# Optimization experiments

Measured on AMD Instinct MI355X. Metric: run time of the kernel, lower is better.

## Reference

```python
import jax, jax.numpy as jnp
import numpy as np

N = 50000          # nodes
E = 1_600_000      # edges (avg degree 32)
F = 64             # num_features == hidden dim of every layer
R = 5              # num_rel (edge ratings)
B = 4              # num_base (basis decomposition)
L = 4              # number of RGCN layers (dim=[64,64,64,64])
K = 2048           # nodes with x[:,0]==1 (target user/item nodes)


def setup_inputs() -> dict:
    key = jax.random.key(0)
    ks = jax.random.split(key, 10)
    x = jax.random.normal(ks[0], (N, F), dtype=jnp.float32)
    target_idx = jnp.arange(K, dtype=jnp.int32)
    # mark exactly K target nodes: x[:,0] == 1 iff node index < K
    col0 = (jnp.arange(N) < K).astype(jnp.float32)
    x = x.at[:, 0].set(col0)
    edge_index = jax.random.randint(ks[1], (2, E), 0, N, dtype=jnp.int32)
    edge_type = jax.random.randint(ks[2], (E,), 0, R, dtype=jnp.int32)
    s = 1.0 / np.sqrt(F)
    bases = jax.random.normal(ks[3], (L, B, F, F), dtype=jnp.float32) * s
    comps = jax.random.normal(ks[4], (L, R, B), dtype=jnp.float32) * (1.0 / np.sqrt(B))
    roots = jax.random.normal(ks[5], (L, F, F), dtype=jnp.float32) * s
    biases = jnp.zeros((L, F), dtype=jnp.float32)
    w1 = jax.random.normal(ks[6], (2 * L * F, 128), dtype=jnp.float32) * (1.0 / np.sqrt(2 * L * F))
    b1 = jnp.zeros((128,), dtype=jnp.float32)
    w2 = jax.random.normal(ks[7], (128, 1), dtype=jnp.float32) * (1.0 / np.sqrt(128))
    b2 = jnp.zeros((1,), dtype=jnp.float32)
    return {"x": x, "edge_index": edge_index, "edge_type": edge_type,
            "target_idx": target_idx, "bases": bases, "comps": comps,
            "roots": roots, "biases": biases, "w1": w1, "b1": b1,
            "w2": w2, "b2": b2}


def _rgcn_layer(x, src, dst, etype, bases_l, comp_l, root_l, bias_l):
    # basis decomposition: W_r = sum_b comp[r,b] * bases[b]   -> [R, in, out]
    W = jnp.einsum('rb,bio->rio', comp_l, bases_l)
    # transform every node under every relation, then gather per edge
    H = jnp.einsum('ni,rio->rno', x, W)          # [R, N, out]
    m = H[etype, src]                            # [E, out] per-edge messages
    # per-(target node, relation) MEAN aggregation (PyG RGCNConv semantics)
    seg = dst * R + etype                        # [E]
    sums = jax.ops.segment_sum(m, seg, num_segments=N * R)
    cnts = jax.ops.segment_sum(jnp.ones((m.shape[0],), dtype=x.dtype), seg,
                               num_segments=N * R)
    mean = sums / jnp.maximum(cnts, 1.0)[:, None]
    agg = mean.reshape(N, R, -1).sum(axis=1)     # sum over relations
    return agg + x @ root_l + bias_l


def reference(x, edge_index, edge_type, target_idx, bases, comps, roots,
              biases, w1, b1, w2, b2):
    # inference mode: edge dropout / feature dropout are identity
    src, dst = edge_index[0], edge_index[1]
    h = x
    h_i = []
    for l in range(L):
        h = jnp.tanh(_rgcn_layer(h, src, dst, edge_type,
                                 bases[l], comps[l], roots[l], biases[l]))
        h_i.append(h)
    h_cat = jnp.concatenate(h_i, axis=1)         # [N, sum(dim)] = [N, 256]
    # u and i masks are identical in the source (x[:,0]==1); target_idx holds
    # exactly those node indices, so index gather == boolean mask selection.
    sel = h_cat[target_idx]                      # [K, 256]
    feat = jnp.concatenate([sel, sel], axis=1)   # [K, 512]
    hid = jax.nn.relu(feat @ w1 + b1)
    out = hid @ w2 + b2
    return out[:, 0]
```

## Files before the change

kernel.cpp:

```cpp
#include <hip/hip_runtime.h>
#include <hip/hip_bf16.h>

#define Nn 50000
#define Ee 1600000
#define Ff 64
#define Rr 5
#define Bb 4
#define Ll 4
#define Kk 2048
#define NBK 196
#define SEGB 1280
#define MsegP (NBK*SEGB)
#define NT16 3125
#define NCH ((Ee+8191)/8192)
#define WTSL (12*4*64*8)

typedef __attribute__((ext_vector_type(8))) short short8;
typedef __attribute__((ext_vector_type(4))) float v4f;

static __device__ __forceinline__ unsigned short f2b(float f){
  unsigned u = __float_as_uint(f);
  unsigned r = (u + 0x7fffu + ((u>>16)&1u)) >> 16;
  return (unsigned short)r;
}
static __device__ __forceinline__ unsigned packbf(float lo, float hi){
  return (unsigned)f2b(lo) | ((unsigned)f2b(hi) << 16);
}
static __device__ __forceinline__ float2 unpackbf(unsigned u){
  return make_float2(__uint_as_float(u << 16), __uint_as_float(u & 0xffff0000u));
}

#define XB_B 6250
#define IV_B (XB_B+196)
#define WE_B (IV_B+128)
#define WS_B (WE_B+48)
#define TF_B (WS_B+13)
#define MS_B (TF_B+1)
__global__ __launch_bounds__(256) void k_setupA(const float* __restrict__ x, unsigned* __restrict__ xb,
    int* __restrict__ inv, const float* __restrict__ w1, float* __restrict__ w1e,
    const float* __restrict__ bases, const float* __restrict__ comps, const float* __restrict__ roots,
    unsigned short* __restrict__ WTs, int* __restrict__ t16f, int* __restrict__ bcnt,
    unsigned* __restrict__ hA, unsigned* __restrict__ hB)
{
  int b = blockIdx.x, t = threadIdx.x;
  if (b < XB_B){
    int idx = b*256 + t;
    int n = idx >> 5, j = idx & 31;
    float2 v = *(const float2*)&x[(size_t)n*64 + 2*j];
    xb[idx] = packbf(v.x, v.y);
  } else if (b < IV_B){
    int i = (b-XB_B)*256 + t;
    if (i < Nn) inv[i] = -1;
  } else if (b < WE_B){
    int idx = (b-IV_B)*256 + t;
    int i = idx >> 7, j = idx & 127;
    w1e[idx] = w1[i*128 + j] + w1[(i+256)*128 + j];
  } else if (b < WS_B){
    int gid = (b-WE_B)*256 + t;
    int lane = gid & 63, nb = (gid>>6)&3, idx2 = gid>>8;
    int l = idx2/12, kk = idx2 - l*12;
    int o = nb*16 + (lane & 15);
    int kbase = kk*32 + (lane>>4)*8;
    const float* basesl = bases + (size_t)l*Bb*Ff*Ff;
    const float* compsl = comps + (size_t)l*Rr*Bb;
    const float* rootsl = roots + (size_t)l*Ff*Ff;
    unsigned short* wp = WTs + (size_t)gid*8;
    #pragma unroll
    for (int j=0;j<8;j++){
      int k = kbase + j;
      float s;
      if (k < 320){
        int c = k >> 6, i = k & 63;
        s = 0.f;
        #pragma unroll
        for (int bb2=0;bb2<Bb;bb2++)
          s += compsl[c*Bb+bb2] * basesl[(bb2*Ff + i)*Ff + o];
      } else {
        s = rootsl[(k-320)*Ff + o];
      }
      wp[j] = f2b(s);
    }
  } else if (b < TF_B){
    int i = (b-WS_B)*256 + t;
    if (i < NT16) t16f[i] = 0;
  } else {
    if (t < NBK+1) bcnt[t] = 0;
    if (t < 32){
      xb[(size_t)Nn*32 + t] = 0;
      hA[(size_t)Nn*32 + t] = 0;
      hB[(size_t)Nn*32 + t] = 0;
    }
  }
}

__global__ __launch_bounds__(256) void k_setupB(const int* __restrict__ tidx, int* __restrict__ inv,
                                                int* __restrict__ t16f){
  int k = blockIdx.x*256+threadIdx.x;
  if (k < Kk){
    int n = tidx[k];
    inv[n] = k;
    t16f[n >> 4] = 1;
  }
}

__global__ __launch_bounds__(256) void k_bcnt(const int* __restrict__ ei, int* __restrict__ bcnt){
  __shared__ int h[NBK];
  int t = threadIdx.x;
  for (int i=t;i<NBK;i+=256) h[i]=0;
  __syncthreads();
  int base = blockIdx.x*8192;
  for (int i=0;i<32;i++){
    int e = base + i*256 + t;
    if (e < Ee) atomicAdd(&h[ei[Ee+e]>>8], 1);
  }
  __syncthreads();
  for (int i=t;i<NBK;i+=256) if (h[i]) atomicAdd(&bcnt[i], h[i]);
}

__global__ __launch_bounds__(256) void k_bscan(const int* __restrict__ bcnt, int* __restrict__ bbase,
                                               int* __restrict__ bfill, int* __restrict__ rowptr){
  __shared__ int s[256];
  int t = threadIdx.x;
  int v = (t < NBK) ? bcnt[t] : 0;
  s[t] = v; __syncthreads();
  #pragma unroll
  for (int off=1; off<256; off<<=1){
    int x = (t>=off) ? s[t-off] : 0;
    __syncthreads();
    s[t] += x;
    __syncthreads();
  }
  if (t < NBK){ int ex = s[t]-v; bbase[t]=ex; bfill[t]=ex; }
  if (t == 0){ bbase[NBK] = Ee; rowptr[MsegP] = Ee; }
}

__global__ __launch_bounds__(256) void k_bin(const int* __restrict__ ei, const int* __restrict__ et,
                                             int* __restrict__ bfill, unsigned* __restrict__ ebin){
  __shared__ unsigned led[8192];
  __shared__ int h[NBK], gb[NBK];
  int t = threadIdx.x;
  for (int i=t;i<NBK;i+=256) h[i]=0;
  __syncthreads();
  int base = blockIdx.x*8192;
  for (int i=0;i<32;i++){
    int e = base + i*256 + t;
    if (e < Ee){
      int src = ei[e];
      int dst = ei[Ee+e];
      int r = et[e];
      led[i*256+t] = (unsigned)src | ((unsigned)(dst&255)<<16) | ((unsigned)r<<24);
      atomicAdd(&h[dst>>8], 1);
    }
  }
  __syncthreads();
  for (int i=t;i<NBK;i+=256) if (h[i]){ gb[i] = atomicAdd(&bfill[i], h[i]); h[i] = 0; }
  __syncthreads();
  for (int i=0;i<32;i++){
    int e = base + i*256 + t;
    if (e < Ee){
      int b = ei[Ee+e]>>8;
      int off = atomicAdd(&h[b], 1);
      ebin[gb[b]+off] = led[i*256+t];
    }
  }
}

__global__ __launch_bounds__(512) void k_sort(const unsigned* __restrict__ ebin, const int* __restrict__ bbase,
                                              unsigned short* __restrict__ srcs, int* __restrict__ rowptr){
  __shared__ int cntA[SEGB], excA[SEGB];
  int b = blockIdx.x, t = threadIdx.x;
  int base = bbase[b], cnt = bbase[b+1]-base;
  for (int i=t;i<SEGB;i+=512) cntA[i]=0;
  __syncthreads();
  for (int i=t;i<cnt;i+=512){
    unsigned u = ebin[base+i];
    int segl = (int)((u>>24)&7u)*256 + (int)((u>>16)&255u);
    atomicAdd(&cntA[segl], 1);
  }
  __syncthreads();
  for (int i=t;i<SEGB;i+=512) excA[i]=cntA[i];
  __syncthreads();
  for (int off=1; off<SEGB; off<<=1){
    int i0=t, i1=t+512, i2=t+1024;
    int v0 = (i0>=off)? excA[i0-off] : 0;
    int v1 = (i1>=off)? excA[i1-off] : 0;
    int v2 = (i2<SEGB && i2>=off)? excA[i2-off] : 0;
    __syncthreads();
    excA[i0]+=v0;
    excA[i1]+=v1;
    if (i2<SEGB) excA[i2]+=v2;
    __syncthreads();
  }
  for (int i=t;i<SEGB;i+=512){
    int ex = excA[i]-cntA[i];
    excA[i] = ex;
    rowptr[b*SEGB+i] = base + ex;
    cntA[i] = 0;
  }
  __syncthreads();
  for (int i=t;i<cnt;i+=512){
    unsigned u = ebin[base+i];
    int segl = (int)((u>>24)&7u)*256 + (int)((u>>16)&255u);
    int off = atomicAdd(&cntA[segl], 1);
    srcs[base + excA[segl] + off] = (unsigned short)(u & 0xffffu);
  }
}

static __device__ __forceinline__ void gpass(int mys, float* A, int p, int half5, int sub, int li,
                                             const unsigned* __restrict__ h2)
{
  int s0 = __shfl(mys, half5 + p +      sub, 64);
  int s1 = __shfl(mys, half5 + p +  4 + sub, 64);
  int s2 = __shfl(mys, half5 + p +  8 + sub, 64);
  int s3 = __shfl(mys, half5 + p + 12 + sub, 64);
  uint4 g0 = *(const uint4*)&h2[(size_t)s0*32 + li*4];
  uint4 g1 = *(const uint4*)&h2[(size_t)s1*32 + li*4];
  uint4 g2 = *(const uint4*)&h2[(size_t)s2*32 + li*4];
  uint4 g3 = *(const uint4*)&h2[(size_t)s3*32 + li*4];
  float2 f;
  f=unpackbf(g0.x); A[0]+=f.x; A[1]+=f.y;  f=unpackbf(g0.y); A[2]+=f.x; A[3]+=f.y;
  f=unpackbf(g0.z); A[4]+=f.x; A[5]+=f.y;  f=unpackbf(g0.w); A[6]+=f.x; A[7]+=f.y;
  f=unpackbf(g1.x); A[0]+=f.x; A[1]+=f.y;  f=unpackbf(g1.y); A[2]+=f.x; A[3]+=f.y;
  f=unpackbf(g1.z); A[4]+=f.x; A[5]+=f.y;  f=unpackbf(g1.w); A[6]+=f.x; A[7]+=f.y;
  f=unpackbf(g2.x); A[0]+=f.x; A[1]+=f.y;  f=unpackbf(g2.y); A[2]+=f.x; A[3]+=f.y;
  f=unpackbf(g2.z); A[4]+=f.x; A[5]+=f.y;  f=unpackbf(g2.w); A[6]+=f.x; A[7]+=f.y;
  f=unpackbf(g3.x); A[0]+=f.x; A[1]+=f.y;  f=unpackbf(g3.y); A[2]+=f.x; A[3]+=f.y;
  f=unpackbf(g3.z); A[4]+=f.x; A[5]+=f.y;  f=unpackbf(g3.w); A[6]+=f.x; A[7]+=f.y;
}

static __device__ __forceinline__ void tail_gather(float* A, int s, int e, int li,
    const unsigned short* __restrict__ srcs, const unsigned* __restrict__ h2)
{
  for (int i = s; i < e; i++){
    uint4 g = *(const uint4*)&h2[(size_t)srcs[i]*32 + li*4];
    float2 f;
    f=unpackbf(g.x); A[0]+=f.x; A[1]+=f.y;  f=unpackbf(g.y); A[2]+=f.x; A[3]+=f.y;
    f=unpackbf(g.z); A[4]+=f.x; A[5]+=f.y;  f=unpackbf(g.w); A[6]+=f.x; A[7]+=f.y;
  }
}

__global__ __launch_bounds__(256, 4) void k_fused(const unsigned short* __restrict__ srcs,
    const int* __restrict__ rowptr, const unsigned* __restrict__ h2,
    const unsigned short* __restrict__ WTsl, const float* __restrict__ bias,
    unsigned short* __restrict__ hn, const int* __restrict__ inv, float* __restrict__ sel,
    int layer, const int* __restrict__ t16f)
{
  if (layer == Ll-1 && t16f[blockIdx.x] == 0) return;
  __shared__ __align__(16) unsigned short ytile[5*16*64];
  char* yb = (char*)ytile;
  int tid = threadIdx.x;
  int hw = tid >> 5;
  int l2 = tid & 31, li = l2 & 7, sub = l2 >> 3;
  int half5 = tid & 32;
  int wl = tid & 63;
  int d0 = blockIdx.x * 16;
  int sbase = (d0 >> 8)*SEGB + (d0 & 255) + hw*2;
  int rl0 = hw*2;

  #pragma unroll 1
  for (int r = 0; r < Rr; ++r){
    int sA = sbase + r*256;
    int2 pp = *(const int2*)&rowptr[sA];
    int p2 = rowptr[sA+2];
    int degA = pp.y - pp.x, degB = p2 - pp.y;
    unsigned ldA = srcs[pp.x + l2];
    unsigned ldB = srcs[pp.y + l2];
    int mysA = (l2 < degA) ? (int)ldA : Nn;
    int mysB = (l2 < degB) ? (int)ldB : Nn;
    float aA[8] = {0.f,0.f,0.f,0.f,0.f,0.f,0.f,0.f};
    float aB[8] = {0.f,0.f,0.f,0.f,0.f,0.f,0.f,0.f};

    gpass(mysA, aA, 0, half5, sub, li, h2);
    gpass(mysB, aB, 0, half5, sub, li, h2);
    if (degA > 16) gpass(mysA, aA, 16, half5, sub, li, h2);
    if (degB > 16) gpass(mysB, aB, 16, half5, sub, li, h2);
    if (sub == 0){
      if (degA > 32) tail_gather(aA, pp.x+32, pp.y, li, srcs, h2);
      if (degB > 32) tail_gather(aB, pp.y+32, p2,   li, srcs, h2);
    }
    #pragma unroll
    for (int k=0;k<8;k++){
      aA[k] += __shfl(aA[k], wl^8, 64);
      aB[k] += __shfl(aB[k], wl^8, 64);
    }
    #pragma unroll
    for (int k=0;k<8;k++){
      aA[k] += __shfl(aA[k], wl^16, 64);
      aB[k] += __shfl(aB[k], wl^16, 64);
    }
    if (sub == 0){
      float scA = (degA > 0) ? 1.0f/(float)degA : 0.f;
      float scB = (degB > 0) ? 1.0f/(float)degB : 0.f;
      uint4 oA, oB;
      oA.x = packbf(aA[0]*scA, aA[1]*scA);
      oA.y = packbf(aA[2]*scA, aA[3]*scA);
      oA.z = packbf(aA[4]*scA, aA[5]*scA);
      oA.w = packbf(aA[6]*scA, aA[7]*scA);
      oB.x = packbf(aB[0]*scB, aB[1]*scB);
      oB.y = packbf(aB[2]*scB, aB[3]*scB);
      oB.z = packbf(aB[4]*scB, aB[5]*scB);
      oB.w = packbf(aB[6]*scB, aB[7]*scB);
      int trA = r*16 + rl0;
      *(uint4*)(yb + (( trA   *128 + li*16) ^ (( rl0   &7)<<4))) = oA;
      *(uint4*)(yb + (((trA+1)*128 + li*16) ^ (((rl0+1)&7)<<4))) = oB;
    }
  }
  __syncthreads();

  int wv = tid >> 6;
  int lane = tid & 63;
  int m = lane & 15, q = lane >> 4;
  const unsigned short* wp = WTsl + (size_t)lane*8 + (size_t)wv*512;
  const char* h2c = (const char*)h2;
  int rowm = d0 + m;
  v4f acc = {0.f,0.f,0.f,0.f};
  #pragma unroll
  for (int kk=0; kk<12; kk++){
    short8 a;
    if (kk < 10){
      int tr = (kk>>1)*16 + m;
      a = *(const short8*)(yb + ((tr*128 + (kk&1)*64 + q*16) ^ ((m&7)<<4)));
    } else {
      a = *(const short8*)(h2c + (size_t)rowm*128 + (size_t)(kk&1)*64 + q*16);
    }
    short8 bf = *(const short8*)(wp + (size_t)kk*2048);
    acc = __builtin_amdgcn_mfma_f32_16x16x32_bf16(a, bf, acc, 0, 0, 0);
  }
  float bc = bias[wv*16 + m];
  #pragma unroll
  for (int j=0;j<4;j++){
    int node = d0 + q*4 + j;
    float rres = tanhf(acc[j] + bc);
    if (layer != Ll-1)
      hn[(size_t)node*64 + wv*16 + m] = f2b(rres);
    int k = inv[node];
    if (k >= 0)
      sel[(size_t)k*256 + layer*64 + wv*16 + m] = rres;
  }
}

__global__ __launch_bounds__(128) void k_mlp(const float* __restrict__ sel, const float* __restrict__ w1e,
    const float* __restrict__ b1, const float* __restrict__ w2, const float* __restrict__ b2,
    float* __restrict__ out)
{
  __shared__ float sfeat[256];
  __shared__ float partial[2];
  int k = blockIdx.x, j = threadIdx.x;
  for (int idx=j; idx<256; idx+=128) sfeat[idx] = sel[(size_t)k*256 + idx];
  __syncthreads();
  float a = b1[j];
  for (int i=0;i<256;i++) a += sfeat[i] * w1e[i*128 + j];
  a = fmaxf(a, 0.f);
  float v = a * w2[j];
  #pragma unroll
  for (int off=32; off>0; off>>=1) v += __shfl_down(v, off, 64);
  if ((j & 63) == 0) partial[j>>6] = v;
  __syncthreads();
  if (j == 0) out[k] = partial[0] + partial[1] + b2[0];
}

extern "C" void kernel_launch(void* const* d_in, const int* in_sizes, int n_in,
                              void* d_out, int out_size, void* d_ws, size_t ws_size,
                              hipStream_t stream){
  const float* x     = (const float*)d_in[0];
  const int*  ei     = (const int*)d_in[1];
  const int*  et     = (const int*)d_in[2];
  const int*  tidx   = (const int*)d_in[3];
  const float* bases = (const float*)d_in[4];
  const float* comps = (const float*)d_in[5];
  const float* roots = (const float*)d_in[6];
  const float* biases= (const float*)d_in[7];
  const float* w1    = (const float*)d_in[8];
  const float* b1    = (const float*)d_in[9];
  const float* w2    = (const float*)d_in[10];
  const float* b2    = (const float*)d_in[11];
  float* out = (float*)d_out;

  char* wsp = (char*)d_ws;
  size_t off = 0;
  auto alloc = [&](size_t bytes)->void*{ void* p = wsp + off; off += (bytes + 255) & ~size_t(255); return p; };
  unsigned* xb    = (unsigned*)alloc(sizeof(unsigned)*((size_t)Nn+1)*32);
  unsigned* hA    = (unsigned*)alloc(sizeof(unsigned)*((size_t)Nn+1)*32);
  unsigned* hB    = (unsigned*)alloc(sizeof(unsigned)*((size_t)Nn+1)*32);
  unsigned* ebin  = (unsigned*)alloc(sizeof(unsigned)*(size_t)Ee);
  int*      bcnt  = (int*)  alloc(sizeof(int)*(NBK+1));
  int*      bbase = (int*)  alloc(sizeof(int)*(NBK+1));
  int*      bfill = (int*)  alloc(sizeof(int)*(NBK));
  int*      rowptr= (int*)  alloc(sizeof(int)*(MsegP+1));
  unsigned short* srcs = (unsigned short*)alloc(sizeof(unsigned short)*((size_t)Ee+64));
  unsigned short* WTs  = (unsigned short*)alloc(sizeof(unsigned short)*(size_t)Ll*WTSL);
  float*    sel   = (float*)alloc(sizeof(float)*(size_t)Kk*256);
  float*    w1e   = (float*)alloc(sizeof(float)*256*128);
  int*      inv   = (int*)  alloc(sizeof(int)*(size_t)Nn);
  int*      t16f  = (int*)  alloc(sizeof(int)*NT16);
  (void)ws_size;

  k_setupA<<<MS_B+1, 256, 0, stream>>>(x, xb, inv, w1, w1e, bases, comps, roots,
                                       WTs, t16f, bcnt, hA, hB);
  k_setupB<<<(Kk+255)/256, 256, 0, stream>>>(tidx, inv, t16f);
  k_bcnt<<<NCH, 256, 0, stream>>>(ei, bcnt);
  k_bscan<<<1, 256, 0, stream>>>(bcnt, bbase, bfill, rowptr);
  k_bin<<<NCH, 256, 0, stream>>>(ei, et, bfill, ebin);
  k_sort<<<NBK, 512, 0, stream>>>(ebin, bbase, srcs, rowptr);

  const unsigned* hc = xb;
  unsigned* hn = hA;
  for (int l=0;l<Ll;l++){
    k_fused<<<NT16, 256, 0, stream>>>(srcs, rowptr, hc, WTs + (size_t)l*WTSL,
                                      biases + (size_t)l*Ff, (unsigned short*)hn,
                                      inv, sel, l, t16f);
    hc = hn;
    hn = (hn == hA) ? hB : hA;
  }
  k_mlp<<<Kk, 128, 0, stream>>>(sel, w1e, b1, w2, b2, out);
}
```

Before: 322.2 us.

## Process 32 nodes per block with 8-lane segment gathers and dual MFMA tiles

The fused RGCN layer kernel now handles 32 destination nodes per block instead of 16. Each (node, relation) segment is gathered by an 8-lane group instead of a 32-lane group with cross-lane reductions, so no shuffle-reduction is needed. The epilogue issues two MFMA tiles that share each weight fragment load, halving the number of blocks and the per-node weight traffic. The catch is loop divergence: each group iterates to the wave's maximum degree, and the doubled shared tile may lower occupancy. Bounds checks are added for the partial last block.

```diff
diff --git a/kernel.cpp b/kernel.cpp
--- a/kernel.cpp
+++ b/kernel.cpp
@@ -11,7 +11,7 @@
 #define NBK 196
 #define SEGB 1280
 #define MsegP (NBK*SEGB)
-#define NT16 3125
+#define NT32 1563
 #define NCH ((Ee+8191)/8192)
 #define WTSL (12*4*64*8)
 
@@ -29,17 +29,23 @@
 static __device__ __forceinline__ float2 unpackbf(unsigned u){
   return make_float2(__uint_as_float(u << 16), __uint_as_float(u & 0xffff0000u));
 }
+static __device__ __forceinline__ void acc8(float* A, uint4 g){
+  float2 f;
+  f=unpackbf(g.x); A[0]+=f.x; A[1]+=f.y;
+  f=unpackbf(g.y); A[2]+=f.x; A[3]+=f.y;
+  f=unpackbf(g.z); A[4]+=f.x; A[5]+=f.y;
+  f=unpackbf(g.w); A[6]+=f.x; A[7]+=f.y;
+}
 
 #define XB_B 6250
 #define IV_B (XB_B+196)
 #define WE_B (IV_B+128)
 #define WS_B (WE_B+48)
-#define TF_B (WS_B+13)
-#define MS_B (TF_B+1)
+#define TF_B (WS_B+7)
 __global__ __launch_bounds__(256) void k_setupA(const float* __restrict__ x, unsigned* __restrict__ xb,
     int* __restrict__ inv, const float* __restrict__ w1, float* __restrict__ w1e,
     const float* __restrict__ bases, const float* __restrict__ comps, const float* __restrict__ roots,
-    unsigned short* __restrict__ WTs, int* __restrict__ t16f, int* __restrict__ bcnt,
+    unsigned short* __restrict__ WTs, int* __restrict__ t32f, int* __restrict__ bcnt,
     unsigned* __restrict__ hA, unsigned* __restrict__ hB)
 {
   int b = blockIdx.x, t = threadIdx.x;
@@ -82,7 +88,7 @@
     }
   } else if (b < TF_B){
     int i = (b-WS_B)*256 + t;
-    if (i < NT16) t16f[i] = 0;
+    if (i < NT32) t32f[i] = 0;
   } else {
     if (t < NBK+1) bcnt[t] = 0;
     if (t < 32){
@@ -94,12 +100,12 @@
 }
 
 __global__ __launch_bounds__(256) void k_setupB(const int* __restrict__ tidx, int* __restrict__ inv,
-                                                int* __restrict__ t16f){
+                                                int* __restrict__ t32f){
   int k = blockIdx.x*256+threadIdx.x;
   if (k < Kk){
     int n = tidx[k];
     inv[n] = k;
-    t16f[n >> 4] = 1;
+    t32f[n >> 5] = 1;
   }
 }
 
@@ -206,104 +212,81 @@
   }
 }
 
-static __device__ __forceinline__ void gpass(int mys, float* A, int p, int half5, int sub, int li,
-                                             const unsigned* __restrict__ h2)
-{
-  int s0 = __shfl(mys, half5 + p +      sub, 64);
-  int s1 = __shfl(mys, half5 + p +  4 + sub, 64);
-  int s2 = __shfl(mys, half5 + p +  8 + sub, 64);
-  int s3 = __shfl(mys, half5 + p + 12 + sub, 64);
-  uint4 g0 = *(const uint4*)&h2[(size_t)s0*32 + li*4];
-  uint4 g1 = *(const uint4*)&h2[(size_t)s1*32 + li*4];
-  uint4 g2 = *(const uint4*)&h2[(size_t)s2*32 + li*4];
-  uint4 g3 = *(const uint4*)&h2[(size_t)s3*32 + li*4];
-  float2 f;
-  f=unpackbf(g0.x); A[0]+=f.x; A[1]+=f.y;  f=unpackbf(g0.y); A[2]+=f.x; A[3]+=f.y;
-  f=unpackbf(g0.z); A[4]+=f.x; A[5]+=f.y;  f=unpackbf(g0.w); A[6]+=f.x; A[7]+=f.y;
-  f=unpackbf(g1.x); A[0]+=f.x; A[1]+=f.y;  f=unpackbf(g1.y); A[2]+=f.x; A[3]+=f.y;
-  f=unpackbf(g1.z); A[4]+=f.x; A[5]+=f.y;  f=unpackbf(g1.w); A[6]+=f.x; A[7]+=f.y;
-  f=unpackbf(g2.x); A[0]+=f.x; A[1]+=f.y;  f=unpackbf(g2.y); A[2]+=f.x; A[3]+=f.y;
-  f=unpackbf(g2.z); A[4]+=f.x; A[5]+=f.y;  f=unpackbf(g2.w); A[6]+=f.x; A[7]+=f.y;
-  f=unpackbf(g3.x); A[0]+=f.x; A[1]+=f.y;  f=unpackbf(g3.y); A[2]+=f.x; A[3]+=f.y;
-  f=unpackbf(g3.z); A[4]+=f.x; A[5]+=f.y;  f=unpackbf(g3.w); A[6]+=f.x; A[7]+=f.y;
-}
-
-static __device__ __forceinline__ void tail_gather(float* A, int s, int e, int li,
-    const unsigned short* __restrict__ srcs, const unsigned* __restrict__ h2)
-{
-  for (int i = s; i < e; i++){
-    uint4 g = *(const uint4*)&h2[(size_t)srcs[i]*32 + li*4];
-    float2 f;
-    f=unpackbf(g.x); A[0]+=f.x; A[1]+=f.y;  f=unpackbf(g.y); A[2]+=f.x; A[3]+=f.y;
-    f=unpackbf(g.z); A[4]+=f.x; A[5]+=f.y;  f=unpackbf(g.w); A[6]+=f.x; A[7]+=f.y;
-  }
-}
-
 __global__ __launch_bounds__(256, 4) void k_fused(const unsigned short* __restrict__ srcs,
     const int* __restrict__ rowptr, const unsigned* __restrict__ h2,
     const unsigned short* __restrict__ WTsl, const float* __restrict__ bias,
     unsigned short* __restrict__ hn, const int* __restrict__ inv, float* __restrict__ sel,
-    int layer, const int* __restrict__ t16f)
+    int layer, const int* __restrict__ t32f)
 {
-  if (layer == Ll-1 && t16f[blockIdx.x] == 0) return;
-  __shared__ __align__(16) unsigned short ytile[5*16*64];
+  if (layer == Ll-1 && t32f[blockIdx.x] == 0) return;
+  __shared__ __align__(16) unsigned short ytile[5*32*64];
   char* yb = (char*)ytile;
   int tid = threadIdx.x;
-  int hw = tid >> 5;
-  int l2 = tid & 31, li = l2 & 7, sub = l2 >> 3;
-  int half5 = tid & 32;
-  int wl = tid & 63;
-  int d0 = blockIdx.x * 16;
-  int sbase = (d0 >> 8)*SEGB + (d0 & 255) + hw*2;
-  int rl0 = hw*2;
+  int grp = tid >> 3;
+  int li  = tid & 7;
+  int grp8 = (tid & 63) & 56;
+  int d0 = blockIdx.x * 32;
+  int segbase = (d0 >> 8)*SEGB + (d0 & 255) + grp;
 
   #pragma unroll 1
   for (int r = 0; r < Rr; ++r){
-    int sA = sbase + r*256;
-    int2 pp = *(const int2*)&rowptr[sA];
-    int p2 = rowptr[sA+2];
-    int degA = pp.y - pp.x, degB = p2 - pp.y;
-    unsigned ldA = srcs[pp.x + l2];
-    unsigned ldB = srcs[pp.y + l2];
-    int mysA = (l2 < degA) ? (int)ldA : Nn;
-    int mysB = (l2 < degB) ? (int)ldB : Nn;
-    float aA[8] = {0.f,0.f,0.f,0.f,0.f,0.f,0.f,0.f};
-    float aB[8] = {0.f,0.f,0.f,0.f,0.f,0.f,0.f,0.f};
-
-    gpass(mysA, aA, 0, half5, sub, li, h2);
-    gpass(mysB, aB, 0, half5, sub, li, h2);
-    if (degA > 16) gpass(mysA, aA, 16, half5, sub, li, h2);
-    if (degB > 16) gpass(mysB, aB, 16, half5, sub, li, h2);
-    if (sub == 0){
-      if (degA > 32) tail_gather(aA, pp.x+32, pp.y, li, srcs, h2);
-      if (degB > 32) tail_gather(aB, pp.y+32, p2,   li, srcs, h2);
-    }
-    #pragma unroll
-    for (int k=0;k<8;k++){
-      aA[k] += __shfl(aA[k], wl^8, 64);
-      aB[k] += __shfl(aB[k], wl^8, 64);
-    }
-    #pragma unroll
-    for (int k=0;k<8;k++){
-      aA[k] += __shfl(aA[k], wl^16, 64);
-      aB[k] += __shfl(aB[k], wl^16, 64);
-    }
-    if (sub == 0){
-      float scA = (degA > 0) ? 1.0f/(float)degA : 0.f;
-      float scB = (degB > 0) ? 1.0f/(float)degB : 0.f;
-      uint4 oA, oB;
-      oA.x = packbf(aA[0]*scA, aA[1]*scA);
-      oA.y = packbf(aA[2]*scA, aA[3]*scA);
-      oA.z = packbf(aA[4]*scA, aA[5]*scA);
-      oA.w = packbf(aA[6]*scA, aA[7]*scA);
-      oB.x = packbf(aB[0]*scB, aB[1]*scB);
-      oB.y = packbf(aB[2]*scB, aB[3]*scB);
-      oB.z = packbf(aB[4]*scB, aB[5]*scB);
-      oB.w = packbf(aB[6]*scB, aB[7]*scB);
-      int trA = r*16 + rl0;
-      *(uint4*)(yb + (( trA   *128 + li*16) ^ (( rl0   &7)<<4))) = oA;
-      *(uint4*)(yb + (((trA+1)*128 + li*16) ^ (((rl0+1)&7)<<4))) = oB;
-    }
+    int seg = segbase + r*256;
+    int s  = rowptr[seg];
+    int e1 = rowptr[seg+1];
+    int deg = e1 - s;
+    unsigned m0 = srcs[s + li];
+    unsigned m1 = srcs[s + 8 + li];
+    int dmax = deg;
+    dmax = max(dmax, __shfl_xor(dmax, 8, 64));
+    dmax = max(dmax, __shfl_xor(dmax, 16, 64));
+    dmax = max(dmax, __shfl_xor(dmax, 32, 64));
+    float A[8] = {0.f,0.f,0.f,0.f,0.f,0.f,0.f,0.f};
+    int j = 0;
+    for (; j+1 < dmax; j += 2){
+      int s0, s1;
+      if (j < 16){
+        unsigned v0 = (j<8)? m0 : m1;
+        s0 = __shfl((int)v0, grp8 + (j&7), 64);
+      } else {
+        s0 = (int)srcs[s+j];
+      }
+      int j1 = j+1;
+      if (j1 < 16){
+        unsigned v1 = (j1<8)? m0 : m1;
+        s1 = __shfl((int)v1, grp8 + (j1&7), 64);
+      } else {
+        s1 = (int)srcs[s+j1];
+      }
+      if (j < deg){
+        uint4 g = *(const uint4*)&h2[(size_t)s0*32 + li*4];
+        acc8(A, g);
+      }
+      if (j1 < deg){
+        uint4 g = *(const uint4*)&h2[(size_t)s1*32 + li*4];
+        acc8(A, g);
+      }
+    }
+    if (j < dmax){
+      int s0;
+      if (j < 16){
+        unsigned v0 = (j<8)? m0 : m1;
+        s0 = __shfl((int)v0, grp8 + (j&7), 64);
+      } else {
+        s0 = (int)srcs[s+j];
+      }
+      if (j < deg){
+        uint4 g = *(const uint4*)&h2[(size_t)s0*32 + li*4];
+        acc8(A, g);
+      }
+    }
+    float sc = (deg > 0) ? 1.0f/(float)deg : 0.f;
+    uint4 o;
+    o.x = packbf(A[0]*sc, A[1]*sc);
+    o.y = packbf(A[2]*sc, A[3]*sc);
+    o.z = packbf(A[4]*sc, A[5]*sc);
+    o.w = packbf(A[6]*sc, A[7]*sc);
+    int tr = r*32 + grp;
+    *(uint4*)(yb + ((tr*128 + li*16) ^ ((tr&7)<<4))) = o;
   }
   __syncthreads();
 
@@ -312,30 +295,42 @@
   int m = lane & 15, q = lane >> 4;
   const unsigned short* wp = WTsl + (size_t)lane*8 + (size_t)wv*512;
   const char* h2c = (const char*)h2;
-  int rowm = d0 + m;
-  v4f acc = {0.f,0.f,0.f,0.f};
+  int row0 = d0 + m, row1 = d0 + 16 + m;
+  int row0c = (row0 < Nn) ? row0 : Nn-1;
+  int row1c = (row1 < Nn) ? row1 : Nn-1;
+  v4f acc0 = {0.f,0.f,0.f,0.f}, acc1 = {0.f,0.f,0.f,0.f};
   #pragma unroll
   for (int kk=0; kk<12; kk++){
-    short8 a;
+    short8 a0, a1;
     if (kk < 10){
-      int tr = (kk>>1)*16 + m;
-      a = *(const short8*)(yb + ((tr*128 + (kk&1)*64 + q*16) ^ ((m&7)<<4)));
+      int rb = (kk>>1)*32;
+      a0 = *(const short8*)(yb + (((rb+m   )*128 + (kk&1)*64 + q*16) ^ ((m&7)<<4)));
+      a1 = *(const short8*)(yb + (((rb+16+m)*128 + (kk&1)*64 + q*16) ^ ((m&7)<<4)));
     } else {
-      a = *(const short8*)(h2c + (size_t)rowm*128 + (size_t)(kk&1)*64 + q*16);
+      a0 = *(const short8*)(h2c + (size_t)row0c*128 + (size_t)(kk&1)*64 + q*16);
+      a1 = *(const short8*)(h2c + (size_t)row1c*128 + (size_t)(kk&1)*64 + q*16);
     }
     short8 bf = *(const short8*)(wp + (size_t)kk*2048);
-    acc = __builtin_amdgcn_mfma_f32_16x16x32_bf16(a, bf, acc, 0, 0, 0);
+    acc0 = __builtin_amdgcn_mfma_f32_16x16x32_bf16(a0, bf, acc0, 0, 0, 0);
+    acc1 = __builtin_amdgcn_mfma_f32_16x16x32_bf16(a1, bf, acc1, 0, 0, 0);
   }
   float bc = bias[wv*16 + m];
   #pragma unroll
   for (int j=0;j<4;j++){
-    int node = d0 + q*4 + j;
-    float rres = tanhf(acc[j] + bc);
-    if (layer != Ll-1)
-      hn[(size_t)node*64 + wv*16 + m] = f2b(rres);
-    int k = inv[node];
-    if (k >= 0)
-      sel[(size_t)k*256 + layer*64 + wv*16 + m] = rres;
+    int node0 = d0 + q*4 + j;
+    int node1 = d0 + 16 + q*4 + j;
+    float r0 = tanhf(acc0[j] + bc);
+    float r1 = tanhf(acc1[j] + bc);
+    if (node0 < Nn){
+      if (layer != Ll-1) hn[(size_t)node0*64 + wv*16 + m] = f2b(r0);
+      int k = inv[node0];
+      if (k >= 0) sel[(size_t)k*256 + layer*64 + wv*16 + m] = r0;
+    }
+    if (node1 < Nn){
+      if (layer != Ll-1) hn[(size_t)node1*64 + wv*16 + m] = f2b(r1);
+      int k = inv[node1];
+      if (k >= 0) sel[(size_t)k*256 + layer*64 + wv*16 + m] = r1;
+    }
   }
 }
 
@@ -392,12 +387,12 @@
   float*    sel   = (float*)alloc(sizeof(float)*(size_t)Kk*256);
   float*    w1e   = (float*)alloc(sizeof(float)*256*128);
   int*      inv   = (int*)  alloc(sizeof(int)*(size_t)Nn);
-  int*      t16f  = (int*)  alloc(sizeof(int)*NT16);
+  int*      t32f  = (int*)  alloc(sizeof(int)*NT32);
   (void)ws_size;
 
-  k_setupA<<<MS_B+1, 256, 0, stream>>>(x, xb, inv, w1, w1e, bases, comps, roots,
-                                       WTs, t16f, bcnt, hA, hB);
-  k_setupB<<<(Kk+255)/256, 256, 0, stream>>>(tidx, inv, t16f);
+  k_setupA<<<TF_B+1, 256, 0, stream>>>(x, xb, inv, w1, w1e, bases, comps, roots,
+                                       WTs, t32f, bcnt, hA, hB);
+  k_setupB<<<(Kk+255)/256, 256, 0, stream>>>(tidx, inv, t32f);
   k_bcnt<<<NCH, 256, 0, stream>>>(ei, bcnt);
   k_bscan<<<1, 256, 0, stream>>>(bcnt, bbase, bfill, rowptr);
   k_bin<<<NCH, 256, 0, stream>>>(ei, et, bfill, ebin);
@@ -406,9 +401,9 @@
   const unsigned* hc = xb;
   unsigned* hn = hA;
   for (int l=0;l<Ll;l++){
-    k_fused<<<NT16, 256, 0, stream>>>(srcs, rowptr, hc, WTs + (size_t)l*WTSL,
+    k_fused<<<NT32, 256, 0, stream>>>(srcs, rowptr, hc, WTs + (size_t)l*WTSL,
                                       biases + (size_t)l*Ff, (unsigned short*)hn,
-                                      inv, sel, l, t16f);
+                                      inv, sel, l, t32f);
     hc = hn;
     hn = (hn == hA) ? hB : hA;
   }
```

After: 313.7 us. 2.6% less time.
